# Performance work log

Measured on AMD Instinct MI355X. Metric: run time of the kernel, lower is better.

## Reference

```python
import jax, jax.numpy as jnp
import numpy as np


def setup_inputs() -> dict:
    key = jax.random.key(0)
    k1, k2 = jax.random.split(key)
    N, C = 2_000_000, 5  # N points, 3 coords + C feature channels
    range_min = jnp.array([0.0, -39.68, -3.0], jnp.float32)
    range_max = jnp.array([69.12, 39.68, 1.0], jnp.float32)
    voxel_size = jnp.array([0.16, 0.16, 4.0], jnp.float32)  # KITTI pillars -> 432x496x1 grid
    xyz = jax.random.uniform(k1, (N, 3), jnp.float32) * (range_max - range_min) + range_min
    feats = jax.random.normal(k2, (N, C), jnp.float32)
    points_feats = jnp.concatenate([xyz, feats], axis=1)
    return {"points_feats": points_feats, "voxel_size": voxel_size,
            "range_min": range_min, "range_max": range_max,
            "max_num_points": 64, "max_voxels": 60000}


def reference(points_feats, voxel_size, range_min, range_max, max_num_points, max_voxels):
    """PointPillars voxelization: hash points into pillars, build dense [V, P, D] tensor.

    Returns fixed-size (padded) outputs for jit-compatibility:
      out_voxels     [max_voxels, max_num_points, D]  zero-padded point feats per voxel
      out_coords     [max_voxels, 3]                  integer voxel coords, order [z, y, x]
      out_num_points [max_voxels]                     points per voxel (0 for unused slots)
    Voxels are ordered canonically by ascending linear cell index; points keep their
    original relative order inside a voxel (stable sort), matching ragged_to_dense+gather
    semantics with zero padding (feats row-0 zero trick in the original).
    """
    N, D = points_feats.shape
    pts = points_feats[:, :3]
    grid = jnp.round((range_max - range_min) / voxel_size).astype(jnp.int32)  # [gx, gy, gz]
    vox = jnp.floor((pts - range_min) / voxel_size).astype(jnp.int32)         # [N, 3] (x, y, z)
    valid = jnp.all((vox >= 0) & (vox < grid), axis=1)
    n_cells = grid[0] * grid[1] * grid[2]
    lin = (vox[:, 2] * grid[1] + vox[:, 1]) * grid[0] + vox[:, 0]
    lin = jnp.where(valid, lin, n_cells)  # invalid points sort to the end

    order = jnp.argsort(lin)  # stable: preserves point order within a voxel
    slin = lin[order]
    svalid = valid[order]
    svox = vox[order]
    sfeats = points_feats[order]

    idx = jnp.arange(N, dtype=jnp.int32)
    is_new = jnp.concatenate([jnp.ones((1,), bool), slin[1:] != slin[:-1]])
    is_start = is_new & svalid                      # first point of each occupied voxel
    voxel_id = jnp.cumsum(is_start.astype(jnp.int32)) - 1
    run_start = jax.lax.cummax(jnp.where(is_start, idx, 0))
    rank = idx - run_start                          # slot of point inside its voxel

    keep = svalid & (voxel_id < max_voxels) & (rank < max_num_points)
    vi = jnp.where(keep, voxel_id, max_voxels)      # out-of-range index -> dropped
    ri = jnp.where(keep, rank, 0)

    out_voxels = jnp.zeros((max_voxels, max_num_points, D), points_feats.dtype)
    out_voxels = out_voxels.at[vi, ri].set(sfeats, mode="drop")

    ci = jnp.where(is_start & (voxel_id < max_voxels), voxel_id, max_voxels)
    out_coords = jnp.zeros((max_voxels, 3), jnp.int32).at[ci].set(svox[:, ::-1], mode="drop")  # [z,y,x]

    out_num_points = jax.ops.segment_sum(keep.astype(jnp.int32), vi,
                                         num_segments=max_voxels + 1)[:max_voxels]
    return out_voxels, out_coords, out_num_points
```

## Files before the change

kernel.cpp:

```cpp
#include <hip/hip_runtime.h>


constexpr int MAXV    = 60000;
constexpr int MAXP    = 64;
constexpr int DF      = 8;
constexpr int NCMAX   = 432 * 496;
constexpr int NB      = NCMAX / 256;
constexpr int EMCAP   = 256;
constexpr int CSTRIDE = 4;
constexpr int CSR_CAP = 1000000;
constexpr int THRESH  = 73728;
constexpr int NBLO    = THRESH / 256;
constexpr int NBHI    = NB - NBLO;

typedef float __attribute__((ext_vector_type(4))) f32x4;

struct Geom { float rm[3], ir[3]; int g[3]; };

__device__ __forceinline__ Geom load_geom(const float* __restrict__ vs,
                                          const float* __restrict__ rmin,
                                          const float* __restrict__ rmax) {
  Geom ge;
#pragma unroll
  for (int a = 0; a < 3; ++a) {
    ge.rm[a] = rmin[a];
    ge.ir[a] = 1.0f / vs[a];
    ge.g[a]  = (int)rintf((rmax[a] - rmin[a]) * ge.ir[a]);
  }
  return ge;
}

__device__ __forceinline__ bool cell_of(float4 p, const Geom& ge, int& lin) {
  float c[3] = { p.x, p.y, p.z };
  int v[3]; bool ok = true;
#pragma unroll
  for (int a = 0; a < 3; ++a) {
    float q = floorf((c[a] - ge.rm[a]) * ge.ir[a]);
    v[a] = (int)q;
    ok = ok && (q >= 0.0f) && (v[a] < ge.g[a]);
  }
  lin = (v[2] * ge.g[1] + v[1]) * ge.g[0] + v[0];
  return ok && lin >= 0 && lin < NCMAX;
}

__global__ void k_count(const float* __restrict__ pts, int N,
                        const float* __restrict__ vs, const float* __restrict__ rmin,
                        const float* __restrict__ rmax,
                        int* __restrict__ counts, unsigned int* __restrict__ linslot) {
  int i = blockIdx.x * blockDim.x + threadIdx.x;
  if (i >= N) return;
  Geom ge = load_geom(vs, rmin, rmax);
  float4 p = *(const float4*)(pts + (size_t)i * DF);
  unsigned int pack = 0xFFFFFFFFu;
  int lin;
  if (cell_of(p, ge, lin) && lin < THRESH) {
    int slot = atomicAdd(counts + (size_t)lin * CSTRIDE, 1);
    pack = ((unsigned int)lin << 8) | (unsigned int)(slot < 255 ? slot : 255);
  }
  linslot[i] = pack;
}

__global__ void k_bsumA(const int* __restrict__ counts, int* __restrict__ bsA,
                        int off) {
  __shared__ int s[256];
  int t = threadIdx.x, b = blockIdx.x + off, i = b * 256 + t;
  s[t] = (counts[(size_t)i * CSTRIDE] > 0) ? 1 : 0;
  __syncthreads();
  for (int o = 128; o > 0; o >>= 1) { if (t < o) s[t] += s[t + o]; __syncthreads(); }
  if (t == 0) bsA[b] = s[0];
}

__global__ void k_fallback(const float* __restrict__ pts, int N,
                           const float* __restrict__ vs, const float* __restrict__ rmin,
                           const float* __restrict__ rmax,
                           int* __restrict__ counts, unsigned int* __restrict__ linslot,
                           const int* __restrict__ bsA) {
  __shared__ int s[256];
  int t = threadIdx.x;
  int v = 0;
  for (int j = t; j < NBLO; j += 256) v += bsA[j];
  s[t] = v; __syncthreads();
  for (int o = 128; o > 0; o >>= 1) { if (t < o) s[t] += s[t + o]; __syncthreads(); }
  if (s[0] >= MAXV) return;
  Geom ge = load_geom(vs, rmin, rmax);
  int t4 = (blockIdx.x * blockDim.x + threadIdx.x) * 4;
  for (int j = 0; j < 4; ++j) {
    int i = t4 + j;
    if (i >= N) break;
    float4 p = *(const float4*)(pts + (size_t)i * DF);
    int lin;
    if (cell_of(p, ge, lin) && lin >= THRESH) {
      int slot = atomicAdd(counts + (size_t)lin * CSTRIDE, 1);
      linslot[i] = ((unsigned int)lin << 8) | (unsigned int)(slot < 255 ? slot : 255);
    }
  }
}

__global__ void k_bsumB(const int* __restrict__ counts, const int* __restrict__ bsA,
                        int* __restrict__ bsB) {
  __shared__ int sp[256];
  __shared__ int s[256];
  int t = threadIdx.x, b = blockIdx.x, i = b * 256 + t;
  int pa = 0;
  for (int j = t; j < b; j += 256) pa += bsA[j];
  sp[t] = pa; __syncthreads();
  for (int off = 128; off > 0; off >>= 1) { if (t < off) sp[t] += sp[t + off]; __syncthreads(); }
  int prefixA = sp[0];
  int cnt = counts[(size_t)i * CSTRIDE];
  int f = (cnt > 0) ? 1 : 0;
  s[t] = f; __syncthreads();
  for (int off = 1; off < 256; off <<= 1) {
    int x = (t >= off) ? s[t - off] : 0;
    __syncthreads(); s[t] += x; __syncthreads();
  }
  int vid = prefixA + s[t] - f;
  int alloc = (f && vid < MAXV) ? min(cnt, EMCAP) : 0;
  __syncthreads();
  s[t] = alloc; __syncthreads();
  for (int off = 128; off > 0; off >>= 1) { if (t < off) s[t] += s[t + off]; __syncthreads(); }
  if (t == 0) bsB[blockIdx.x] = s[0];
}

__global__ void k_final(const int* __restrict__ counts, const int* __restrict__ bsA,
                        const int* __restrict__ bsB,
                        int* __restrict__ cellbase, int* __restrict__ vbase,
                        int* __restrict__ vcnt,
                        float* __restrict__ out_coords, float* __restrict__ out_nump) {
  __shared__ int sp[256], so[256], sk[256];
  int t = threadIdx.x, b = blockIdx.x, i = b * 256 + t;
  int pa = 0, pb = 0;
  for (int j = t; j < b; j += 256) { pa += bsA[j]; pb += bsB[j]; }
  sp[t] = pa; __syncthreads();
  for (int off = 128; off > 0; off >>= 1) { if (t < off) sp[t] += sp[t + off]; __syncthreads(); }
  int prefixA = sp[0]; __syncthreads();
  sp[t] = pb; __syncthreads();
  for (int off = 128; off > 0; off >>= 1) { if (t < off) sp[t] += sp[t + off]; __syncthreads(); }
  int prefixB = sp[0];
  int cnt = counts[(size_t)i * CSTRIDE];
  int f = (cnt > 0) ? 1 : 0;
  so[t] = f; __syncthreads();
  for (int off = 1; off < 256; off <<= 1) {
    int x = (t >= off) ? so[t - off] : 0;
    __syncthreads(); so[t] += x; __syncthreads();
  }
  int vid = prefixA + so[t] - f;
  int alloc = (f && vid < MAXV) ? min(cnt, EMCAP) : 0;
  sk[t] = alloc; __syncthreads();
  for (int off = 1; off < 256; off <<= 1) {
    int x = (t >= off) ? sk[t - off] : 0;
    __syncthreads(); sk[t] += x; __syncthreads();
  }
  int base = prefixB + sk[t] - alloc;
  if (alloc > 0) {
    cellbase[i] = base;
    vbase[vid] = base;
    vcnt[vid] = alloc;
    int x = i % 432, rest = i / 432, y = rest % 496, z = rest / 496;
    out_coords[(size_t)vid * 3 + 0] = (float)z;
    out_coords[(size_t)vid * 3 + 1] = (float)y;
    out_coords[(size_t)vid * 3 + 2] = (float)x;
    out_nump[vid] = (float)(cnt < MAXP ? cnt : MAXP);
  } else {
    cellbase[i] = -1;
  }
}

__global__ void k_scatter(const unsigned int* __restrict__ linslot, int N,
                          const int* __restrict__ cellbase, int* __restrict__ csr) {
  int t4 = (blockIdx.x * blockDim.x + threadIdx.x) * 4;
  if (t4 + 3 >= N) {
    for (int i = t4; i < N; ++i) {
      unsigned int pk = linslot[i];
      if (pk == 0xFFFFFFFFu) continue;
      int lin = (int)(pk >> 8), sl = (int)(pk & 255u);
      int b = cellbase[lin];
      if (b < 0 || sl >= EMCAP) continue;
      int pos = b + sl;
      if (pos < CSR_CAP) csr[pos] = i;
    }
    return;
  }
  uint4 pk4 = *(const uint4*)(linslot + t4);
  unsigned int pk[4] = { pk4.x, pk4.y, pk4.z, pk4.w };
#pragma unroll
  for (int j = 0; j < 4; ++j) {
    if (pk[j] == 0xFFFFFFFFu) continue;
    int lin = (int)(pk[j] >> 8), sl = (int)(pk[j] & 255u);
    int b = cellbase[lin];
    if (b < 0 || sl >= EMCAP) continue;
    int pos = b + sl;
    if (pos < CSR_CAP) csr[pos] = t4 + j;
  }
}

__global__ void __launch_bounds__(64)
k_emit(const float* __restrict__ pts,
       const int* __restrict__ vbase, const int* __restrict__ vcnt,
       const int* __restrict__ csr, float* __restrict__ out_vox) {
  int v = blockIdx.x, t = threadIdx.x;
  int kf = vcnt[v];
  __shared__ int sidx[EMCAP];
  __shared__ int sorted[MAXP];
  sorted[t] = -1;
  int base = vbase[v];
  for (int j = t; j < kf; j += 64) sidx[j] = csr[base + j];
  __syncthreads();
  for (int e = t; e < kf; e += 64) {
    int my = sidx[e], rank = 0;
    for (int j = 0; j < kf; ++j) rank += (sidx[j] < my) ? 1 : 0;
    if (rank < MAXP) sorted[rank] = my;
  }
  __syncthreads();
  int pi = sorted[t];
  f32x4 a = {0.f, 0.f, 0.f, 0.f};
  f32x4 b = {0.f, 0.f, 0.f, 0.f};
  if (pi >= 0) {
    const f32x4* src = (const f32x4*)(pts + (size_t)pi * DF);
    a = src[0]; b = src[1];
  }
  f32x4* dst = (f32x4*)(out_vox + ((size_t)v * MAXP + t) * DF);
  __builtin_nontemporal_store(a, dst);
  __builtin_nontemporal_store(b, dst + 1);
}

extern "C" void kernel_launch(void* const* d_in, const int* in_sizes, int n_in,
                              void* d_out, int out_size, void* d_ws, size_t ws_size,
                              hipStream_t stream) {
  const float* pts  = (const float*)d_in[0];
  const float* vs   = (const float*)d_in[1];
  const float* rmin = (const float*)d_in[2];
  const float* rmax = (const float*)d_in[3];
  const int N = in_sizes[0] / DF;

  char* ws = (char*)d_ws;
  int* counts          = (int*)(ws);
  int* vcnt            = (int*)(ws +  3428352);
  int* vbase           = (int*)(ws +  3668352);
  int* bsA             = (int*)(ws +  3908352);
  int* bsB             = (int*)(ws +  3912448);
  int* cellbase        = (int*)(ws +  3916544);
  unsigned int* linslot= (unsigned int*)(ws + 4773632);
  int* csr             = (int*)(ws + 12773632);

  float* out_vox    = (float*)d_out;
  float* out_coords = (float*)d_out + (size_t)MAXV * MAXP * DF;
  float* out_nump   = out_coords + (size_t)MAXV * 3;

  hipMemsetAsync(ws, 0, 3908352, stream);
  hipMemsetAsync((void*)out_coords, 0, (size_t)MAXV * 4 * 4, stream);

  const int nb1 = (N + 255) / 256;
  const int nb4 = (N + 1023) / 1024;
  k_count   <<<nb1, 256, 0, stream>>>(pts, N, vs, rmin, rmax, counts, linslot);
  k_bsumA   <<<NBLO, 256, 0, stream>>>(counts, bsA, 0);
  k_fallback<<<nb4, 256, 0, stream>>>(pts, N, vs, rmin, rmax, counts, linslot, bsA);
  k_bsumA   <<<NBHI, 256, 0, stream>>>(counts, bsA, NBLO);
  k_bsumB   <<<NB, 256, 0, stream>>>(counts, bsA, bsB);
  k_final   <<<NB, 256, 0, stream>>>(counts, bsA, bsB, cellbase, vbase, vcnt,
                                     out_coords, out_nump);
  k_scatter <<<nb4, 256, 0, stream>>>(linslot, N, cellbase, csr);
  k_emit    <<<MAXV, 64, 0, stream>>>(pts, vbase, vcnt, csr, out_vox);
}
```

Measured before the change: 244.8 us.

## Fuse scan kernels into single-pass decoupled-lookback scan and batch emit voxels

```diff
diff --git a/kernel.cpp b/kernel.cpp
--- a/kernel.cpp
+++ b/kernel.cpp
@@ -9,9 +9,8 @@
 constexpr int EMCAP   = 256;
 constexpr int CSTRIDE = 4;
 constexpr int CSR_CAP = 1000000;
-constexpr int THRESH  = 73728;
+constexpr int THRESH  = 61440;
 constexpr int NBLO    = THRESH / 256;
-constexpr int NBHI    = NB - NBLO;
 
 typedef float __attribute__((ext_vector_type(4))) f32x4;
 
@@ -60,14 +59,13 @@
   linslot[i] = pack;
 }
 
-__global__ void k_bsumA(const int* __restrict__ counts, int* __restrict__ bsA,
-                        int off) {
+__global__ void k_bsumA(const int* __restrict__ counts, int* __restrict__ bsA) {
   __shared__ int s[256];
-  int t = threadIdx.x, b = blockIdx.x + off, i = b * 256 + t;
+  int t = threadIdx.x, i = blockIdx.x * 256 + t;
   s[t] = (counts[(size_t)i * CSTRIDE] > 0) ? 1 : 0;
   __syncthreads();
   for (int o = 128; o > 0; o >>= 1) { if (t < o) s[t] += s[t + o]; __syncthreads(); }
-  if (t == 0) bsA[b] = s[0];
+  if (t == 0) bsA[blockIdx.x] = s[0];
 }
 
 __global__ void k_fallback(const float* __restrict__ pts, int N,
@@ -96,61 +94,81 @@
   }
 }
 
-__global__ void k_bsumB(const int* __restrict__ counts, const int* __restrict__ bsA,
-                        int* __restrict__ bsB) {
-  __shared__ int sp[256];
+__device__ __forceinline__ int lookback64(unsigned* st, int b, int t) {
+  int excl = 0;
+  int j = b - 1;
+  while (j >= 0) {
+    int idx = j - t;
+    unsigned s;
+    do {
+      s = __hip_atomic_load(&st[idx < 0 ? 0 : idx], __ATOMIC_RELAXED,
+                            __HIP_MEMORY_SCOPE_AGENT);
+      if (idx < 0) s = 2u << 30;
+    } while (s < (1u << 30));
+    unsigned long long pf = __ballot(s >= (2u << 30));
+    int L = (pf != 0ULL) ? (__ffsll((unsigned long long)pf) - 1) : 64;
+    int contrib = (t <= L) ? (int)(s & 0x3FFFFFFFu) : 0;
+    for (int o = 32; o > 0; o >>= 1) contrib += __shfl_down(contrib, o);
+    if (t == 0) excl += contrib;
+    if (L < 64) break;
+    j -= 64;
+  }
+  return excl;
+}
+
+__global__ void __launch_bounds__(256)
+k_fused(const int* __restrict__ counts,
+        unsigned* __restrict__ stA, unsigned* __restrict__ stB,
+        int* __restrict__ cellbase, int* __restrict__ vbase,
+        int* __restrict__ vcnt,
+        float* __restrict__ out_coords, float* __restrict__ out_nump) {
   __shared__ int s[256];
+  __shared__ int sh[2];
   int t = threadIdx.x, b = blockIdx.x, i = b * 256 + t;
-  int pa = 0;
-  for (int j = t; j < b; j += 256) pa += bsA[j];
-  sp[t] = pa; __syncthreads();
-  for (int off = 128; off > 0; off >>= 1) { if (t < off) sp[t] += sp[t + off]; __syncthreads(); }
-  int prefixA = sp[0];
   int cnt = counts[(size_t)i * CSTRIDE];
   int f = (cnt > 0) ? 1 : 0;
   s[t] = f; __syncthreads();
-  for (int off = 1; off < 256; off <<= 1) {
-    int x = (t >= off) ? s[t - off] : 0;
+  for (int o = 1; o < 256; o <<= 1) {
+    int x = (t >= o) ? s[t - o] : 0;
     __syncthreads(); s[t] += x; __syncthreads();
   }
-  int vid = prefixA + s[t] - f;
+  int fscan = s[t];
+  int ftot  = s[255];
+  if (t == 0)
+    __hip_atomic_store(&stA[b], (1u << 30) | (unsigned)ftot,
+                       __ATOMIC_RELAXED, __HIP_MEMORY_SCOPE_AGENT);
+  if (t < 64) {
+    int e = lookback64(stA, b, t);
+    if (t == 0) {
+      __hip_atomic_store(&stA[b], (2u << 30) | (unsigned)(e + ftot),
+                         __ATOMIC_RELAXED, __HIP_MEMORY_SCOPE_AGENT);
+      sh[0] = e;
+    }
+  }
+  __syncthreads();
+  int prefixA = sh[0];
+  int vid = prefixA + fscan - f;
   int alloc = (f && vid < MAXV) ? min(cnt, EMCAP) : 0;
-  __syncthreads();
   s[t] = alloc; __syncthreads();
-  for (int off = 128; off > 0; off >>= 1) { if (t < off) s[t] += s[t + off]; __syncthreads(); }
-  if (t == 0) bsB[blockIdx.x] = s[0];
-}
-
-__global__ void k_final(const int* __restrict__ counts, const int* __restrict__ bsA,
-                        const int* __restrict__ bsB,
-                        int* __restrict__ cellbase, int* __restrict__ vbase,
-                        int* __restrict__ vcnt,
-                        float* __restrict__ out_coords, float* __restrict__ out_nump) {
-  __shared__ int sp[256], so[256], sk[256];
-  int t = threadIdx.x, b = blockIdx.x, i = b * 256 + t;
-  int pa = 0, pb = 0;
-  for (int j = t; j < b; j += 256) { pa += bsA[j]; pb += bsB[j]; }
-  sp[t] = pa; __syncthreads();
-  for (int off = 128; off > 0; off >>= 1) { if (t < off) sp[t] += sp[t + off]; __syncthreads(); }
-  int prefixA = sp[0]; __syncthreads();
-  sp[t] = pb; __syncthreads();
-  for (int off = 128; off > 0; off >>= 1) { if (t < off) sp[t] += sp[t + off]; __syncthreads(); }
-  int prefixB = sp[0];
-  int cnt = counts[(size_t)i * CSTRIDE];
-  int f = (cnt > 0) ? 1 : 0;
-  so[t] = f; __syncthreads();
-  for (int off = 1; off < 256; off <<= 1) {
-    int x = (t >= off) ? so[t - off] : 0;
-    __syncthreads(); so[t] += x; __syncthreads();
-  }
-  int vid = prefixA + so[t] - f;
-  int alloc = (f && vid < MAXV) ? min(cnt, EMCAP) : 0;
-  sk[t] = alloc; __syncthreads();
-  for (int off = 1; off < 256; off <<= 1) {
-    int x = (t >= off) ? sk[t - off] : 0;
-    __syncthreads(); sk[t] += x; __syncthreads();
-  }
-  int base = prefixB + sk[t] - alloc;
+  for (int o = 1; o < 256; o <<= 1) {
+    int x = (t >= o) ? s[t - o] : 0;
+    __syncthreads(); s[t] += x; __syncthreads();
+  }
+  int ascan = s[t];
+  int atot  = s[255];
+  if (t == 0)
+    __hip_atomic_store(&stB[b], (1u << 30) | (unsigned)atot,
+                       __ATOMIC_RELAXED, __HIP_MEMORY_SCOPE_AGENT);
+  if (t < 64) {
+    int e = lookback64(stB, b, t);
+    if (t == 0) {
+      __hip_atomic_store(&stB[b], (2u << 30) | (unsigned)(e + atot),
+                         __ATOMIC_RELAXED, __HIP_MEMORY_SCOPE_AGENT);
+      sh[1] = e;
+    }
+  }
+  __syncthreads();
+  int base = sh[1] + ascan - alloc;
   if (alloc > 0) {
     cellbase[i] = base;
     vbase[vid] = base;
@@ -193,25 +211,26 @@
   }
 }
 
-__global__ void __launch_bounds__(64)
+__global__ void __launch_bounds__(256)
 k_emit(const float* __restrict__ pts,
        const int* __restrict__ vbase, const int* __restrict__ vcnt,
        const int* __restrict__ csr, float* __restrict__ out_vox) {
-  int v = blockIdx.x, t = threadIdx.x;
+  int w = threadIdx.x >> 6, t = threadIdx.x & 63;
+  int v = blockIdx.x * 4 + w;
+  __shared__ int sidx[4][EMCAP];
+  __shared__ int sorted[4][MAXP];
   int kf = vcnt[v];
-  __shared__ int sidx[EMCAP];
-  __shared__ int sorted[MAXP];
-  sorted[t] = -1;
   int base = vbase[v];
-  for (int j = t; j < kf; j += 64) sidx[j] = csr[base + j];
+  sorted[w][t] = -1;
+  for (int j = t; j < kf; j += 64) sidx[w][j] = csr[base + j];
   __syncthreads();
   for (int e = t; e < kf; e += 64) {
-    int my = sidx[e], rank = 0;
-    for (int j = 0; j < kf; ++j) rank += (sidx[j] < my) ? 1 : 0;
-    if (rank < MAXP) sorted[rank] = my;
-  }
-  __syncthreads();
-  int pi = sorted[t];
+    int my = sidx[w][e], rank = 0;
+    for (int j = 0; j < kf; ++j) rank += (sidx[w][j] < my) ? 1 : 0;
+    if (rank < MAXP) sorted[w][rank] = my;
+  }
+  __syncthreads();
+  int pi = sorted[w][t];
   f32x4 a = {0.f, 0.f, 0.f, 0.f};
   f32x4 b = {0.f, 0.f, 0.f, 0.f};
   if (pi >= 0) {
@@ -237,27 +256,26 @@
   int* vcnt            = (int*)(ws +  3428352);
   int* vbase           = (int*)(ws +  3668352);
   int* bsA             = (int*)(ws +  3908352);
-  int* bsB             = (int*)(ws +  3912448);
-  int* cellbase        = (int*)(ws +  3916544);
-  unsigned int* linslot= (unsigned int*)(ws + 4773632);
-  int* csr             = (int*)(ws + 12773632);
+  unsigned* stA        = (unsigned*)(ws + 3912448);
+  unsigned* stB        = (unsigned*)(ws + 3916544);
+  int* cellbase        = (int*)(ws +  3920640);
+  unsigned int* linslot= (unsigned int*)(ws + 4777728);
+  int* csr             = (int*)(ws + 12777728);
 
   float* out_vox    = (float*)d_out;
   float* out_coords = (float*)d_out + (size_t)MAXV * MAXP * DF;
   float* out_nump   = out_coords + (size_t)MAXV * 3;
 
-  hipMemsetAsync(ws, 0, 3908352, stream);
+  hipMemsetAsync(ws, 0, 3920640, stream);
   hipMemsetAsync((void*)out_coords, 0, (size_t)MAXV * 4 * 4, stream);
 
   const int nb1 = (N + 255) / 256;
   const int nb4 = (N + 1023) / 1024;
   k_count   <<<nb1, 256, 0, stream>>>(pts, N, vs, rmin, rmax, counts, linslot);
-  k_bsumA   <<<NBLO, 256, 0, stream>>>(counts, bsA, 0);
+  k_bsumA   <<<NBLO, 256, 0, stream>>>(counts, bsA);
   k_fallback<<<nb4, 256, 0, stream>>>(pts, N, vs, rmin, rmax, counts, linslot, bsA);
-  k_bsumA   <<<NBHI, 256, 0, stream>>>(counts, bsA, NBLO);
-  k_bsumB   <<<NB, 256, 0, stream>>>(counts, bsA, bsB);
-  k_final   <<<NB, 256, 0, stream>>>(counts, bsA, bsB, cellbase, vbase, vcnt,
+  k_fused   <<<NB, 256, 0, stream>>>(counts, stA, stB, cellbase, vbase, vcnt,
                                      out_coords, out_nump);
   k_scatter <<<nb4, 256, 0, stream>>>(linslot, N, cellbase, csr);
-  k_emit    <<<MAXV, 64, 0, stream>>>(pts, vbase, vcnt, csr, out_vox);
-}
+  k_emit    <<<MAXV / 4, 256, 0, stream>>>(pts, vbase, vcnt, csr, out_vox);
+}
```

After: 246.6 us. Within noise of the previous version (+0.7%).
